# Optimization experiments

Measured on AMD Instinct MI355X. Metric: run time of the kernel, lower is better.

## Reference

```python
import jax, jax.numpy as jnp
import numpy as np


def setup_inputs() -> dict:
    key = jax.random.key(0)
    ks = jax.random.split(key, 8)
    B, H, C, K, D, E, CW = 128, 100, 32, 4, 400, 200, 100
    N = B * C
    return {
        "his": jax.random.normal(ks[0], (B, H, K, D), jnp.float32),
        "cdd": jax.random.normal(ks[1], (B, C, K, D), jnp.float32),
        "channel_weight": jax.random.normal(ks[2], (N, K, CW), jnp.float32),
        "W_att": jax.random.normal(ks[3], (K, D, E), jnp.float32) * (1.0 / np.sqrt(D)),
        "b_att": jnp.zeros((K, E), jnp.float32),
        "q_att": jax.random.uniform(ks[4], (K, E), jnp.float32, -0.1, 0.1),
        "W_lin": jax.random.normal(ks[5], (D + CW, E), jnp.float32) * (1.0 / np.sqrt(D + CW)),
        "b_lin": jnp.zeros((E,), jnp.float32),
        "q_vec": jax.random.uniform(ks[6], (E,), jnp.float32, -0.1, 0.1),
    }


def reference(his, cdd, channel_weight, W_att, b_att, q_att, W_lin, b_lin, q_vec):
    B, H, K, D = his.shape
    C = cdd.shape[1]
    N = B * C

    # Per-channel additive attention over history (AdditiveAttention1 per k).
    # The original repeats his over the C candidates before attending, but the
    # attention result is independent of the candidate, so compute once per B.
    t = jnp.tanh(jnp.einsum("bhkd,kde->bkhe", his, W_att) + b_att[None, :, None, :])  # [B,K,H,E]
    a = jax.nn.softmax(jnp.einsum("bkhe,ke->bkh", t, q_att), axis=-1)                 # [B,K,H]
    u_b = jnp.einsum("bkh,bhkd->bkd", a, his)                                          # [B,K,D]

    # Broadcast to [B*C, K, D] (matches torch's repeat+view).
    u_channel = jnp.broadcast_to(u_b[:, None], (B, C, K, D)).reshape(N, K, D)

    # Per-channel candidate score: dot(u_k, cdd_k).
    cdd_flat = cdd.reshape(N, K, D)
    score = jnp.einsum("nkd,nkd->nk", u_channel, cdd_flat)[..., None]  # [N,K,1]

    # Channel-combination attention: linear + tanh + softmax over K.
    cw = jnp.concatenate([u_channel, channel_weight], axis=-1)          # [N,K,D+100]
    temp = jnp.tanh(jnp.einsum("nkf,fe->nke", cw, W_lin) + b_lin)       # [N,K,E]
    cand_w = jax.nn.softmax(jnp.einsum("nke,e->nk", temp, q_vec), axis=1)  # [N,K]

    scores = jnp.einsum("nk,nk->n", cand_w, score[..., 0])[:, None]     # [N,1]
    return scores, u_channel
```

## Files before the change

kernel.cpp:

```cpp
#include <hip/hip_runtime.h>
#include <hip/hip_bf16.h>
#include <math.h>

#define B_ 128
#define H_ 100
#define C_ 32
#define K_ 4
#define D_ 400
#define E_ 200
#define CW_ 100
#define N_ (B_*C_)
#define NCH 13
#define NTI 13
#define MR_ 112

typedef short bf16x8 __attribute__((ext_vector_type(8)));
typedef float f32x4  __attribute__((ext_vector_type(4)));

__device__ __forceinline__ short f2b(float f) {
  union { float f; unsigned u; } x; x.f = f;
  unsigned r = x.u + 0x7fffu + ((x.u >> 16) & 1u);
  return (short)(r >> 16);
}

__device__ __forceinline__ void gload_lds16(const void* g, void* l) {
  __builtin_amdgcn_global_load_lds((const __attribute__((address_space(1))) void*)g,
                                   (__attribute__((address_space(3))) void*)l, 16, 0, 0);
}

__global__ __launch_bounds__(256) void k0_cast(const float* __restrict__ W_att,
                                               short* __restrict__ WT) {
  const int k = blockIdx.x, c = blockIdx.y;
  const int tid = threadIdx.x;
  __shared__ float Wst[32][200];
  for (int idx = tid; idx < 32*200; idx += 256) {
    const int j = idx / 200, col = idx % 200;
    const int d = c*32 + j;
    Wst[j][col] = (d < D_) ? W_att[((size_t)k*D_ + d)*E_ + col] : 0.f;
  }
  __syncthreads();
  short* dst = WT + (size_t)(k*NCH + c)*208*40;
  for (int idx = tid; idx < 208*40; idx += 256) {
    const int col = idx / 40, j = idx % 40;
    const float v = (col < E_ && j < 32) ? Wst[j][col] : 0.f;
    dst[idx] = f2b(v);
  }
}

__global__ __launch_bounds__(512) void k12_fused(const float* __restrict__ his,
                                                 const short* __restrict__ WT,
                                                 const float* __restrict__ b_att,
                                                 const float* __restrict__ q_att,
                                                 const float* __restrict__ W_lin,
                                                 const float* __restrict__ b_lin,
                                                 float* __restrict__ u_b,
                                                 float* __restrict__ ulin) {
  const int b = blockIdx.x, k = blockIdx.y;
  const int tid = threadIdx.x;
  const int w = tid >> 6, l = tid & 63;
  const int ln16 = l & 15, g = l >> 4;

  __shared__ __align__(16) short Al[2][MR_][40];
  __shared__ __align__(16) short Bl[2][208][40];
  __shared__ float sl[MR_];
  __shared__ float sv[128];
  __shared__ float sa[H_];
  __shared__ float4 part[4][100];
  __shared__ float ul[D_];

  f32x4 acc[NTI];
  #pragma unroll
  for (int nt = 0; nt < NTI; ++nt) acc[nt] = (f32x4){0.f, 0.f, 0.f, 0.f};

  const int arow = tid >> 2, aq = tid & 3;
  const bool astage = (tid < 448);
  const float* hisrow = his + (((size_t)b*H_ + arow)*K_ + k)*D_;
  const short* WTk = WT + (size_t)k*NCH*208*40;

  float4 a0, a1;
  {
    const int d = 0 + aq*8;
    a0 = (float4){0,0,0,0}; a1 = a0;
    if (astage && arow < H_ && d < D_) {
      a0 = *(const float4*)(hisrow + d);
      a1 = *(const float4*)(hisrow + d + 4);
    }
    const short* src = WTk;
    for (int i = tid; i < 1040; i += 512)
      gload_lds16(src + i*8, (short*)&Bl[0][0][0] + i*8);
    if (astage) {
      short s8[8];
      s8[0]=f2b(a0.x); s8[1]=f2b(a0.y); s8[2]=f2b(a0.z); s8[3]=f2b(a0.w);
      s8[4]=f2b(a1.x); s8[5]=f2b(a1.y); s8[6]=f2b(a1.z); s8[7]=f2b(a1.w);
      *(bf16x8*)&Al[0][arow][aq*8] = *(bf16x8*)s8;
    }
  }
  __syncthreads();

  int buf = 0;
  for (int c = 0; c < NCH; ++c) {
    const int nb = buf ^ 1;
    const bool more = (c + 1 < NCH);
    if (more) {
      const int d = (c+1)*32 + aq*8;
      a0 = (float4){0,0,0,0}; a1 = a0;
      if (astage && arow < H_ && d < D_) {
        a0 = *(const float4*)(hisrow + d);
        a1 = *(const float4*)(hisrow + d + 4);
      }
      const short* src = WTk + (size_t)(c+1)*208*40;
      for (int i = tid; i < 1040; i += 512)
        gload_lds16(src + i*8, (short*)&Bl[nb][0][0] + i*8);
    }
    if (w < 7) {
      const bf16x8 af = *(const bf16x8*)&Al[buf][w*16 + ln16][g*8];
      #pragma unroll
      for (int nt = 0; nt < NTI; ++nt) {
        const bf16x8 bf = *(const bf16x8*)&Bl[buf][nt*16 + ln16][g*8];
        acc[nt] = __builtin_amdgcn_mfma_f32_16x16x32_bf16(af, bf, acc[nt], 0, 0, 0);
      }
    }
    if (more && astage) {
      short s8[8];
      s8[0]=f2b(a0.x); s8[1]=f2b(a0.y); s8[2]=f2b(a0.z); s8[3]=f2b(a0.w);
      s8[4]=f2b(a1.x); s8[5]=f2b(a1.y); s8[6]=f2b(a1.z); s8[7]=f2b(a1.w);
      *(bf16x8*)&Al[nb][arow][aq*8] = *(bf16x8*)s8;
    }
    __syncthreads();
    buf = nb;
  }

  if (w < 7) {
    float p[4] = {0.f, 0.f, 0.f, 0.f};
    #pragma unroll
    for (int nt = 0; nt < NTI; ++nt) {
      const int e = nt*16 + ln16;
      float q = 0.f, bb = 0.f;
      if (e < E_) { q = q_att[k*E_ + e]; bb = b_att[k*E_ + e]; }
      #pragma unroll
      for (int reg = 0; reg < 4; ++reg)
        p[reg] += tanhf(acc[nt][reg] + bb) * q;
    }
    #pragma unroll
    for (int off = 1; off < 16; off <<= 1)
      #pragma unroll
      for (int reg = 0; reg < 4; ++reg) p[reg] += __shfl_xor(p[reg], off);
    if (ln16 == 0) {
      #pragma unroll
      for (int reg = 0; reg < 4; ++reg) sl[w*16 + g*4 + reg] = p[reg];
    }
  }
  __syncthreads();

  const float v = (tid < H_) ? sl[tid] : -INFINITY;
  if (tid < 128) sv[tid] = v;
  __syncthreads();
  for (int s = 64; s > 0; s >>= 1) { if (tid < s) sv[tid] = fmaxf(sv[tid], sv[tid+s]); __syncthreads(); }
  const float mx = sv[0];
  __syncthreads();
  const float ev = (tid < H_) ? expf(v - mx) : 0.f;
  if (tid < 128) sv[tid] = ev;
  __syncthreads();
  for (int s = 64; s > 0; s >>= 1) { if (tid < s) sv[tid] += sv[tid+s]; __syncthreads(); }
  const float inv = 1.f / sv[0];
  if (tid < H_) sa[tid] = ev * inv;
  __syncthreads();

  const int gg = tid / 100, d4 = tid % 100;
  if (tid < 400) {
    float4 a4 = {0.f, 0.f, 0.f, 0.f};
    const float* hp = his + (((size_t)b*H_ + gg*25)*K_ + k)*D_ + d4*4;
    #pragma unroll 5
    for (int h = 0; h < 25; ++h) {
      const float4 x = *(const float4*)(hp + (size_t)h*K_*D_);
      const float ww = sa[gg*25 + h];
      a4.x += ww*x.x; a4.y += ww*x.y; a4.z += ww*x.z; a4.w += ww*x.w;
    }
    part[gg][d4] = a4;
  }
  __syncthreads();
  if (tid < 100) {
    const float4 p0 = part[0][tid], p1 = part[1][tid], p2 = part[2][tid], p3 = part[3][tid];
    float4 a4;
    a4.x = p0.x+p1.x+p2.x+p3.x; a4.y = p0.y+p1.y+p2.y+p3.y;
    a4.z = p0.z+p1.z+p2.z+p3.z; a4.w = p0.w+p1.w+p2.w+p3.w;
    *(float4*)&ul[tid*4] = a4;
    *(float4*)(u_b + ((size_t)b*K_ + k)*D_ + tid*4) = a4;
  }
  __syncthreads();

  if (tid < E_) {
    float c0 = b_lin[tid], c1 = 0.f, c2 = 0.f, c3 = 0.f;
    #pragma unroll 2
    for (int d = 0; d < D_; d += 4) {
      c0 += ul[d]   * W_lin[(size_t)d*E_     + tid];
      c1 += ul[d+1] * W_lin[(size_t)(d+1)*E_ + tid];
      c2 += ul[d+2] * W_lin[(size_t)(d+2)*E_ + tid];
      c3 += ul[d+3] * W_lin[(size_t)(d+3)*E_ + tid];
    }
    ulin[((size_t)b*K_ + k)*E_ + tid] = c0 + c1 + c2 + c3;
  }
}

__global__ __launch_bounds__(256) void k4_score(const float* __restrict__ cdd,
                                                const float* __restrict__ cwt,
                                                const float* __restrict__ W_lin,
                                                const float* __restrict__ q_vec,
                                                const float* __restrict__ u_b,
                                                const float* __restrict__ ulin,
                                                float* __restrict__ out) {
  const int n = blockIdx.x;
  const int b = n >> 5;
  const int tid = threadIdx.x;
  const int wv = tid >> 6, ln = tid & 63;
  __shared__ float cw[K_][CW_];
  __shared__ float red[4][K_];
  __shared__ float sc[K_];

  for (int idx = tid; idx < K_*CW_; idx += 256)
    cw[idx / CW_][idx % CW_] = cwt[(size_t)n*K_*CW_ + idx];
  __syncthreads();

  {
    const float4* up = (const float4*)(u_b + ((size_t)b*K_ + wv)*D_);
    const float4* cp = (const float4*)(cdd + ((size_t)n*K_ + wv)*D_);
    float s = 0.f;
    for (int dd = ln; dd < 100; dd += 64) {
      const float4 u = up[dd], c = cp[dd];
      s += u.x*c.x + u.y*c.y + u.z*c.z + u.w*c.w;
    }
    #pragma unroll
    for (int off = 32; off >= 1; off >>= 1) s += __shfl_down(s, off);
    if (ln == 0) sc[wv] = s;
  }

  float pl0 = 0.f, pl1 = 0.f, pl2 = 0.f, pl3 = 0.f;
  if (tid < E_) {
    const int e = tid;
    float a0 = 0.f, a1 = 0.f, a2 = 0.f, a3 = 0.f;
    #pragma unroll 4
    for (int c = 0; c < CW_; ++c) {
      const float w = W_lin[(size_t)(D_ + c)*E_ + e];
      a0 += cw[0][c]*w; a1 += cw[1][c]*w; a2 += cw[2][c]*w; a3 += cw[3][c]*w;
    }
    const float q = q_vec[e];
    const float* ue = ulin + (size_t)b*K_*E_ + e;
    pl0 = tanhf(ue[0*E_] + a0) * q;
    pl1 = tanhf(ue[1*E_] + a1) * q;
    pl2 = tanhf(ue[2*E_] + a2) * q;
    pl3 = tanhf(ue[3*E_] + a3) * q;
  }
  #pragma unroll
  for (int off = 1; off < 64; off <<= 1) {
    pl0 += __shfl_xor(pl0, off); pl1 += __shfl_xor(pl1, off);
    pl2 += __shfl_xor(pl2, off); pl3 += __shfl_xor(pl3, off);
  }
  if (ln == 0) { red[wv][0] = pl0; red[wv][1] = pl1; red[wv][2] = pl2; red[wv][3] = pl3; }
  __syncthreads();

  if (tid == 0) {
    const float l0 = red[0][0]+red[1][0]+red[2][0]+red[3][0];
    const float l1 = red[0][1]+red[1][1]+red[2][1]+red[3][1];
    const float l2 = red[0][2]+red[1][2]+red[2][2]+red[3][2];
    const float l3 = red[0][3]+red[1][3]+red[2][3]+red[3][3];
    const float m = fmaxf(fmaxf(l0, l1), fmaxf(l2, l3));
    const float e0 = expf(l0 - m), e1 = expf(l1 - m);
    const float e2 = expf(l2 - m), e3 = expf(l3 - m);
    const float s = e0 + e1 + e2 + e3;
    out[n] = (e0*sc[0] + e1*sc[1] + e2*sc[2] + e3*sc[3]) / s;
  }

  {
    const float4* ub4 = (const float4*)(u_b + (size_t)b*K_*D_);
    float4* uo = (float4*)(out + N_ + (size_t)n*K_*D_);
    for (int idx = tid; idx < 400; idx += 256) uo[idx] = ub4[idx];
  }
}

extern "C" void kernel_launch(void* const* d_in, const int* in_sizes, int n_in,
                              void* d_out, int out_size, void* d_ws, size_t ws_size,
                              hipStream_t stream) {
  const float* his   = (const float*)d_in[0];
  const float* cdd   = (const float*)d_in[1];
  const float* cwt   = (const float*)d_in[2];
  const float* W_att = (const float*)d_in[3];
  const float* b_att = (const float*)d_in[4];
  const float* q_att = (const float*)d_in[5];
  const float* W_lin = (const float*)d_in[6];
  const float* b_lin = (const float*)d_in[7];
  const float* q_vec = (const float*)d_in[8];
  float* out = (float*)d_out;

  float* ws   = (float*)d_ws;
  float* u_b  = ws;
  float* ulin = u_b + (size_t)B_*K_*D_;
  short* WT   = (short*)(ulin + (size_t)B_*K_*E_);

  k0_cast  <<<dim3(K_, NCH),  256, 0, stream>>>(W_att, WT);
  k12_fused<<<dim3(B_, K_),   512, 0, stream>>>(his, WT, b_att, q_att, W_lin, b_lin, u_b, ulin);
  k4_score <<<N_,             256, 0, stream>>>(cdd, cwt, W_lin, q_vec, u_b, ulin, out);
}
```

Before: 252.2 us.

## Use 32x32 MFMA tiles, split W_lin GEMV, and batch four rows per score block

The attention GEMM moves from 16x16x32 to 32x32x16 MFMA with a 2D wave tiling, zero-padded LDS tiles, and a manually unrolled double-buffer loop. The projection GEMV is split over 400 threads with a shared-memory reduction. The score kernel now handles four candidate rows per block, reusing each W_lin load across four rows and issuing fewer blocks. This raises register and LDS pressure in exchange for more reuse and fewer launches of small blocks.

```diff
diff --git a/kernel.cpp b/kernel.cpp
--- a/kernel.cpp
+++ b/kernel.cpp
@@ -11,11 +11,10 @@
 #define CW_ 100
 #define N_ (B_*C_)
 #define NCH 13
-#define NTI 13
 #define MR_ 112
 
 typedef short bf16x8 __attribute__((ext_vector_type(8)));
-typedef float f32x4  __attribute__((ext_vector_type(4)));
+typedef float f32x16 __attribute__((ext_vector_type(16)));
 
 __device__ __forceinline__ short f2b(float f) {
   union { float f; unsigned u; } x; x.f = f;
@@ -47,112 +46,135 @@
   }
 }
 
-__global__ __launch_bounds__(512) void k12_fused(const float* __restrict__ his,
-                                                 const short* __restrict__ WT,
-                                                 const float* __restrict__ b_att,
-                                                 const float* __restrict__ q_att,
-                                                 const float* __restrict__ W_lin,
-                                                 const float* __restrict__ b_lin,
-                                                 float* __restrict__ u_b,
-                                                 float* __restrict__ ulin) {
+__global__ __launch_bounds__(512, 4) void k12_fused(const float* __restrict__ his,
+                                                    const short* __restrict__ WT,
+                                                    const float* __restrict__ b_att,
+                                                    const float* __restrict__ q_att,
+                                                    const float* __restrict__ W_lin,
+                                                    const float* __restrict__ b_lin,
+                                                    float* __restrict__ u_b,
+                                                    float* __restrict__ ulin) {
   const int b = blockIdx.x, k = blockIdx.y;
   const int tid = threadIdx.x;
   const int w = tid >> 6, l = tid & 63;
-  const int ln16 = l & 15, g = l >> 4;
-
-  __shared__ __align__(16) short Al[2][MR_][40];
-  __shared__ __align__(16) short Bl[2][208][40];
-  __shared__ float sl[MR_];
+  const int wm = w >> 1, wn = w & 1;
+  const int ln32 = l & 31, hi = l >> 5;
+  const int koct8 = hi * 8;
+
+  __shared__ __align__(16) short Al[2][128][40];
+  __shared__ __align__(16) short Bl[2][224][40];
+  __shared__ float slp[2][MR_];
   __shared__ float sv[128];
   __shared__ float sa[H_];
   __shared__ float4 part[4][100];
   __shared__ float ul[D_];
-
-  f32x4 acc[NTI];
+  __shared__ float ulp[2][E_];
+
+  f32x16 acc[4];
   #pragma unroll
-  for (int nt = 0; nt < NTI; ++nt) acc[nt] = (f32x4){0.f, 0.f, 0.f, 0.f};
+  for (int t = 0; t < 4; ++t) acc[t] = (f32x16)(0.f);
+
+  for (int i = tid; i < 16*40; i += 512) {
+    const int r = i / 40, j = i % 40;
+    Al[0][112 + r][j] = 0; Al[1][112 + r][j] = 0;
+    Bl[0][208 + r][j] = 0; Bl[1][208 + r][j] = 0;
+  }
 
   const int arow = tid >> 2, aq = tid & 3;
   const bool astage = (tid < 448);
   const float* hisrow = his + (((size_t)b*H_ + arow)*K_ + k)*D_;
-  const short* WTk = WT + (size_t)k*NCH*208*40;
-
-  float4 a0, a1;
+  const short* WTk = WT + (size_t)k*NCH*8320;
+  const int arow32 = wm*32 + ln32;
+  const float4 zf4 = {0.f, 0.f, 0.f, 0.f};
+
+#define ISSUE_A(cidx, r0, r1)                                           \
+  { r0 = zf4; r1 = zf4;                                                 \
+    const int d_ = (cidx)*32 + aq*8;                                    \
+    if (astage && arow < H_ && d_ < D_) {                               \
+      r0 = *(const float4*)(hisrow + d_);                               \
+      r1 = *(const float4*)(hisrow + d_ + 4);                           \
+    } }
+
+#define CONV_A(bufdst, r0, r1)                                          \
+  if (astage) {                                                         \
+    short s8[8];                                                        \
+    s8[0]=f2b(r0.x); s8[1]=f2b(r0.y); s8[2]=f2b(r0.z); s8[3]=f2b(r0.w); \
+    s8[4]=f2b(r1.x); s8[5]=f2b(r1.y); s8[6]=f2b(r1.z); s8[7]=f2b(r1.w); \
+    *(bf16x8*)&Al[bufdst][arow][aq*8] = *(bf16x8*)s8;                   \
+  }
+
+#define DMA_B(cidx, bufdst)                                             \
+  { const short* src_ = WTk + (size_t)(cidx)*8320;                      \
+    for (int i_ = tid; i_ < 1040; i_ += 512)                            \
+      gload_lds16(src_ + i_*8, (short*)&Bl[bufdst][0][0] + i_*8); }
+
+#define COMPUTE(bufc)                                                   \
+  { const bf16x8 af0 = *(const bf16x8*)&Al[bufc][arow32][koct8];        \
+    const bf16x8 af1 = *(const bf16x8*)&Al[bufc][arow32][16 + koct8];   \
+    _Pragma("unroll")                                                   \
+    for (int t = 0; t < 4; ++t) {                                       \
+      if (2*t + wn < 7) {                                               \
+        const int col = (wn + 2*t)*32 + ln32;                           \
+        const bf16x8 bf0 = *(const bf16x8*)&Bl[bufc][col][koct8];       \
+        acc[t] = __builtin_amdgcn_mfma_f32_32x32x16_bf16(af0, bf0, acc[t], 0, 0, 0); \
+        const bf16x8 bf1 = *(const bf16x8*)&Bl[bufc][col][16 + koct8];  \
+        acc[t] = __builtin_amdgcn_mfma_f32_32x32x16_bf16(af1, bf1, acc[t], 0, 0, 0); \
+      } } }
+
+  float4 pa0, pa1, pb0, pb1;
+  ISSUE_A(0, pa0, pa1);
+  ISSUE_A(1, pb0, pb1);
+  DMA_B(0, 0);
+  CONV_A(0, pa0, pa1);
+  __syncthreads();
+
+  for (int c = 0; c < NCH; c += 2) {
+    if (c + 2 < NCH) ISSUE_A(c+2, pa0, pa1);
+    if (c + 1 < NCH) DMA_B(c+1, 1);
+    COMPUTE(0);
+    if (c + 1 < NCH) { CONV_A(1, pb0, pb1); __syncthreads(); }
+    if (c + 1 < NCH) {
+      if (c + 3 < NCH) ISSUE_A(c+3, pb0, pb1);
+      if (c + 2 < NCH) DMA_B(c+2, 0);
+      COMPUTE(1);
+      if (c + 2 < NCH) { CONV_A(0, pa0, pa1); __syncthreads(); }
+    }
+  }
+
   {
-    const int d = 0 + aq*8;
-    a0 = (float4){0,0,0,0}; a1 = a0;
-    if (astage && arow < H_ && d < D_) {
-      a0 = *(const float4*)(hisrow + d);
-      a1 = *(const float4*)(hisrow + d + 4);
-    }
-    const short* src = WTk;
-    for (int i = tid; i < 1040; i += 512)
-      gload_lds16(src + i*8, (short*)&Bl[0][0][0] + i*8);
-    if (astage) {
-      short s8[8];
-      s8[0]=f2b(a0.x); s8[1]=f2b(a0.y); s8[2]=f2b(a0.z); s8[3]=f2b(a0.w);
-      s8[4]=f2b(a1.x); s8[5]=f2b(a1.y); s8[6]=f2b(a1.z); s8[7]=f2b(a1.w);
-      *(bf16x8*)&Al[0][arow][aq*8] = *(bf16x8*)s8;
-    }
-  }
-  __syncthreads();
-
-  int buf = 0;
-  for (int c = 0; c < NCH; ++c) {
-    const int nb = buf ^ 1;
-    const bool more = (c + 1 < NCH);
-    if (more) {
-      const int d = (c+1)*32 + aq*8;
-      a0 = (float4){0,0,0,0}; a1 = a0;
-      if (astage && arow < H_ && d < D_) {
-        a0 = *(const float4*)(hisrow + d);
-        a1 = *(const float4*)(hisrow + d + 4);
+    float p[16];
+    #pragma unroll
+    for (int r = 0; r < 16; ++r) p[r] = 0.f;
+    #pragma unroll
+    for (int t = 0; t < 4; ++t) {
+      if (2*t + wn < 7) {
+        const int e = (wn + 2*t)*32 + ln32;
+        if (e < E_) {
+          const float q  = q_att[k*E_ + e];
+          const float bb = b_att[k*E_ + e];
+          #pragma unroll
+          for (int r = 0; r < 16; ++r) {
+            const int row = wm*32 + (r&3) + 8*(r>>2) + 4*hi;
+            if (row < H_) p[r] += tanhf(acc[t][r] + bb) * q;
+          }
+        }
       }
-      const short* src = WTk + (size_t)(c+1)*208*40;
-      for (int i = tid; i < 1040; i += 512)
-        gload_lds16(src + i*8, (short*)&Bl[nb][0][0] + i*8);
-    }
-    if (w < 7) {
-      const bf16x8 af = *(const bf16x8*)&Al[buf][w*16 + ln16][g*8];
-      #pragma unroll
-      for (int nt = 0; nt < NTI; ++nt) {
-        const bf16x8 bf = *(const bf16x8*)&Bl[buf][nt*16 + ln16][g*8];
-        acc[nt] = __builtin_amdgcn_mfma_f32_16x16x32_bf16(af, bf, acc[nt], 0, 0, 0);
+    }
+    #pragma unroll
+    for (int off = 1; off < 32; off <<= 1)
+      #pragma unroll
+      for (int r = 0; r < 16; ++r) p[r] += __shfl_xor(p[r], off);
+    if (ln32 == 0) {
+      #pragma unroll
+      for (int r = 0; r < 16; ++r) {
+        const int row = wm*32 + (r&3) + 8*(r>>2) + 4*hi;
+        if (row < MR_) slp[wn][row] = p[r];
       }
     }
-    if (more && astage) {
-      short s8[8];
-      s8[0]=f2b(a0.x); s8[1]=f2b(a0.y); s8[2]=f2b(a0.z); s8[3]=f2b(a0.w);
-      s8[4]=f2b(a1.x); s8[5]=f2b(a1.y); s8[6]=f2b(a1.z); s8[7]=f2b(a1.w);
-      *(bf16x8*)&Al[nb][arow][aq*8] = *(bf16x8*)s8;
-    }
-    __syncthreads();
-    buf = nb;
-  }
-
-  if (w < 7) {
-    float p[4] = {0.f, 0.f, 0.f, 0.f};
-    #pragma unroll
-    for (int nt = 0; nt < NTI; ++nt) {
-      const int e = nt*16 + ln16;
-      float q = 0.f, bb = 0.f;
-      if (e < E_) { q = q_att[k*E_ + e]; bb = b_att[k*E_ + e]; }
-      #pragma unroll
-      for (int reg = 0; reg < 4; ++reg)
-        p[reg] += tanhf(acc[nt][reg] + bb) * q;
-    }
-    #pragma unroll
-    for (int off = 1; off < 16; off <<= 1)
-      #pragma unroll
-      for (int reg = 0; reg < 4; ++reg) p[reg] += __shfl_xor(p[reg], off);
-    if (ln16 == 0) {
-      #pragma unroll
-      for (int reg = 0; reg < 4; ++reg) sl[w*16 + g*4 + reg] = p[reg];
-    }
-  }
-  __syncthreads();
-
-  const float v = (tid < H_) ? sl[tid] : -INFINITY;
+  }
+  __syncthreads();
+
+  const float v = (tid < H_) ? slp[0][tid] + slp[1][tid] : -INFINITY;
   if (tid < 128) sv[tid] = v;
   __syncthreads();
   for (int s = 64; s > 0; s >>= 1) { if (tid < s) sv[tid] = fmaxf(sv[tid], sv[tid+s]); __syncthreads(); }
@@ -189,17 +211,22 @@
   }
   __syncthreads();
 
-  if (tid < E_) {
-    float c0 = b_lin[tid], c1 = 0.f, c2 = 0.f, c3 = 0.f;
+  if (tid < 400) {
+    const int dg = tid / 200, e = tid % 200;
+    const int dbase = dg * 200;
+    float c0 = 0.f, c1 = 0.f, c2 = 0.f, c3 = 0.f;
     #pragma unroll 2
-    for (int d = 0; d < D_; d += 4) {
-      c0 += ul[d]   * W_lin[(size_t)d*E_     + tid];
-      c1 += ul[d+1] * W_lin[(size_t)(d+1)*E_ + tid];
-      c2 += ul[d+2] * W_lin[(size_t)(d+2)*E_ + tid];
-      c3 += ul[d+3] * W_lin[(size_t)(d+3)*E_ + tid];
-    }
-    ulin[((size_t)b*K_ + k)*E_ + tid] = c0 + c1 + c2 + c3;
-  }
+    for (int d = 0; d < 200; d += 4) {
+      c0 += ul[dbase+d]   * W_lin[(size_t)(dbase+d)*E_     + e];
+      c1 += ul[dbase+d+1] * W_lin[(size_t)(dbase+d+1)*E_ + e];
+      c2 += ul[dbase+d+2] * W_lin[(size_t)(dbase+d+2)*E_ + e];
+      c3 += ul[dbase+d+3] * W_lin[(size_t)(dbase+d+3)*E_ + e];
+    }
+    ulp[dg][e] = c0 + c1 + c2 + c3;
+  }
+  __syncthreads();
+  if (tid < E_)
+    ulin[((size_t)b*K_ + k)*E_ + tid] = ulp[0][tid] + ulp[1][tid] + b_lin[tid];
 }
 
 __global__ __launch_bounds__(256) void k4_score(const float* __restrict__ cdd,
@@ -209,71 +236,101 @@
                                                 const float* __restrict__ u_b,
                                                 const float* __restrict__ ulin,
                                                 float* __restrict__ out) {
-  const int n = blockIdx.x;
-  const int b = n >> 5;
+  const int n0 = blockIdx.x * 4;
+  const int b  = n0 >> 5;
   const int tid = threadIdx.x;
   const int wv = tid >> 6, ln = tid & 63;
-  __shared__ float cw[K_][CW_];
-  __shared__ float red[4][K_];
-  __shared__ float sc[K_];
-
-  for (int idx = tid; idx < K_*CW_; idx += 256)
-    cw[idx / CW_][idx % CW_] = cwt[(size_t)n*K_*CW_ + idx];
-  __syncthreads();
+  __shared__ float cw[4][K_][CW_];
+  __shared__ float red[4][4][K_];
+  __shared__ float sc[4][K_];
 
   {
-    const float4* up = (const float4*)(u_b + ((size_t)b*K_ + wv)*D_);
-    const float4* cp = (const float4*)(cdd + ((size_t)n*K_ + wv)*D_);
-    float s = 0.f;
-    for (int dd = ln; dd < 100; dd += 64) {
-      const float4 u = up[dd], c = cp[dd];
-      s += u.x*c.x + u.y*c.y + u.z*c.z + u.w*c.w;
-    }
-    #pragma unroll
-    for (int off = 32; off >= 1; off >>= 1) s += __shfl_down(s, off);
-    if (ln == 0) sc[wv] = s;
-  }
-
-  float pl0 = 0.f, pl1 = 0.f, pl2 = 0.f, pl3 = 0.f;
+    const float4* src = (const float4*)(cwt + (size_t)n0*K_*CW_);
+    float4* dst = (float4*)&cw[0][0][0];
+    for (int idx = tid; idx < 400; idx += 256) dst[idx] = src[idx];
+  }
+  __syncthreads();
+
+  {
+    const float4* up = (const float4*)(u_b + (size_t)b*K_*D_);
+    const float4* cp = (const float4*)(cdd + (size_t)(n0 + wv)*K_*D_);
+    #pragma unroll
+    for (int kk = 0; kk < K_; ++kk) {
+      float s = 0.f;
+      for (int dd = ln; dd < 100; dd += 64) {
+        const float4 u = up[kk*100 + dd], c = cp[kk*100 + dd];
+        s += u.x*c.x + u.y*c.y + u.z*c.z + u.w*c.w;
+      }
+      #pragma unroll
+      for (int off = 32; off >= 1; off >>= 1) s += __shfl_down(s, off);
+      if (ln == 0) sc[wv][kk] = s;
+    }
+  }
+
+  float pl[4][K_];
+  #pragma unroll
+  for (int n4 = 0; n4 < 4; ++n4)
+    #pragma unroll
+    for (int kk = 0; kk < K_; ++kk) pl[n4][kk] = 0.f;
+
   if (tid < E_) {
     const int e = tid;
-    float a0 = 0.f, a1 = 0.f, a2 = 0.f, a3 = 0.f;
-    #pragma unroll 4
+    float a[4][K_];
+    #pragma unroll
+    for (int n4 = 0; n4 < 4; ++n4)
+      #pragma unroll
+      for (int kk = 0; kk < K_; ++kk) a[n4][kk] = 0.f;
+    #pragma unroll 2
     for (int c = 0; c < CW_; ++c) {
-      const float w = W_lin[(size_t)(D_ + c)*E_ + e];
-      a0 += cw[0][c]*w; a1 += cw[1][c]*w; a2 += cw[2][c]*w; a3 += cw[3][c]*w;
+      const float wlc = W_lin[(size_t)(D_ + c)*E_ + e];
+      #pragma unroll
+      for (int n4 = 0; n4 < 4; ++n4)
+        #pragma unroll
+        for (int kk = 0; kk < K_; ++kk)
+          a[n4][kk] += cw[n4][kk][c] * wlc;
     }
     const float q = q_vec[e];
-    const float* ue = ulin + (size_t)b*K_*E_ + e;
-    pl0 = tanhf(ue[0*E_] + a0) * q;
-    pl1 = tanhf(ue[1*E_] + a1) * q;
-    pl2 = tanhf(ue[2*E_] + a2) * q;
-    pl3 = tanhf(ue[3*E_] + a3) * q;
+    float ue[K_];
+    #pragma unroll
+    for (int kk = 0; kk < K_; ++kk) ue[kk] = ulin[((size_t)b*K_ + kk)*E_ + e];
+    #pragma unroll
+    for (int n4 = 0; n4 < 4; ++n4)
+      #pragma unroll
+      for (int kk = 0; kk < K_; ++kk)
+        pl[n4][kk] = tanhf(ue[kk] + a[n4][kk]) * q;
   }
   #pragma unroll
-  for (int off = 1; off < 64; off <<= 1) {
-    pl0 += __shfl_xor(pl0, off); pl1 += __shfl_xor(pl1, off);
-    pl2 += __shfl_xor(pl2, off); pl3 += __shfl_xor(pl3, off);
-  }
-  if (ln == 0) { red[wv][0] = pl0; red[wv][1] = pl1; red[wv][2] = pl2; red[wv][3] = pl3; }
-  __syncthreads();
-
-  if (tid == 0) {
-    const float l0 = red[0][0]+red[1][0]+red[2][0]+red[3][0];
-    const float l1 = red[0][1]+red[1][1]+red[2][1]+red[3][1];
-    const float l2 = red[0][2]+red[1][2]+red[2][2]+red[3][2];
-    const float l3 = red[0][3]+red[1][3]+red[2][3]+red[3][3];
-    const float m = fmaxf(fmaxf(l0, l1), fmaxf(l2, l3));
-    const float e0 = expf(l0 - m), e1 = expf(l1 - m);
-    const float e2 = expf(l2 - m), e3 = expf(l3 - m);
+  for (int off = 1; off < 64; off <<= 1)
+    #pragma unroll
+    for (int n4 = 0; n4 < 4; ++n4)
+      #pragma unroll
+      for (int kk = 0; kk < K_; ++kk) pl[n4][kk] += __shfl_xor(pl[n4][kk], off);
+  if (ln == 0) {
+    #pragma unroll
+    for (int n4 = 0; n4 < 4; ++n4)
+      #pragma unroll
+      for (int kk = 0; kk < K_; ++kk) red[wv][n4][kk] = pl[n4][kk];
+  }
+  __syncthreads();
+
+  if (tid < 4) {
+    float lg[K_];
+    #pragma unroll
+    for (int kk = 0; kk < K_; ++kk)
+      lg[kk] = red[0][tid][kk] + red[1][tid][kk] + red[2][tid][kk] + red[3][tid][kk];
+    const float m = fmaxf(fmaxf(lg[0], lg[1]), fmaxf(lg[2], lg[3]));
+    const float e0 = expf(lg[0]-m), e1 = expf(lg[1]-m);
+    const float e2 = expf(lg[2]-m), e3 = expf(lg[3]-m);
     const float s = e0 + e1 + e2 + e3;
-    out[n] = (e0*sc[0] + e1*sc[1] + e2*sc[2] + e3*sc[3]) / s;
+    out[n0 + tid] = (e0*sc[tid][0] + e1*sc[tid][1] + e2*sc[tid][2] + e3*sc[tid][3]) / s;
   }
 
   {
     const float4* ub4 = (const float4*)(u_b + (size_t)b*K_*D_);
-    float4* uo = (float4*)(out + N_ + (size_t)n*K_*D_);
-    for (int idx = tid; idx < 400; idx += 256) uo[idx] = ub4[idx];
+    for (int idx = tid; idx < 1600; idx += 256) {
+      const int n4 = idx / 400, off = idx % 400;
+      *((float4*)(out + N_ + (size_t)(n0 + n4)*K_*D_) + off) = ub4[off];
+    }
   }
 }
 
@@ -298,5 +355,5 @@
 
   k0_cast  <<<dim3(K_, NCH),  256, 0, stream>>>(W_att, WT);
   k12_fused<<<dim3(B_, K_),   512, 0, stream>>>(his, WT, b_att, q_att, W_lin, b_lin, u_b, ulin);
-  k4_score <<<N_,             256, 0, stream>>>(cdd, cwt, W_lin, q_vec, u_b, ulin, out);
-}
+  k4_score <<<N_/4,           256, 0, stream>>>(cdd, cwt, W_lin, q_vec, u_b, ulin, out);
+}
```

Result: faster. 244.4 us (-3.1%).
